# Performance work log

Measured on AMD Instinct MI355X. Metric: run time of the kernel, lower is better.

## Reference

```python
import jax, jax.numpy as jnp
import numpy as np

NS, NI, NC, C, E, M = 50000, 20000, 1000, 128, 1000000, 250000


def setup_inputs() -> dict:
    key = jax.random.key(0)
    ks = jax.random.split(key, 12)
    xavier = (2.0 / (C + C)) ** 0.5  # xavier_normal_ std for square weight
    return {
        "stu_x": jax.random.normal(ks[0], (NS, C), jnp.float32),
        "item_x": jax.random.normal(ks[1], (NI, C), jnp.float32),
        "conc_x": jax.random.normal(ks[2], (NC, C), jnp.float32),
        "W_stu": jax.random.normal(ks[3], (C, C), jnp.float32) * xavier,
        "b_stu": jnp.zeros((C,), jnp.float32),
        "W_item": jax.random.normal(ks[4], (C, C), jnp.float32) * xavier,
        "b_item": jnp.zeros((C,), jnp.float32),
        "W_pred": jax.random.normal(ks[5], (1, C), jnp.float32) * ((2.0 / (1 + C)) ** 0.5),
        "b_pred": jnp.zeros((1,), jnp.float32),
        "stu_track": jax.random.randint(ks[6], (E,), 0, NS, jnp.int32),
        "item_index": jax.random.randint(ks[7], (E,), 0, NI, jnp.int32),
        "conc_index": jax.random.randint(ks[8], (E,), 0, NC, jnp.int32),
        "mean_index": jax.random.randint(ks[9], (E,), 0, M, jnp.int32),
        "num_segments": M,
    }


def _segment_mean(vals, seg_ids, num_segments):
    sums = jax.ops.segment_sum(vals, seg_ids, num_segments=num_segments)
    cnt = jax.ops.segment_sum(jnp.ones((vals.shape[0], 1), vals.dtype), seg_ids,
                              num_segments=num_segments)
    return sums / jnp.maximum(cnt, 1.0)


def reference(stu_x, item_x, conc_x, W_stu, b_stu, W_item, b_item, W_pred, b_pred,
              stu_track, item_index, conc_index, mean_index, num_segments):
    # Feature (stu): shared lin_l=lin_r; aggregate is identity -> per-edge output
    conc_s = conc_x @ W_stu.T          # [NC, C] projected source (concepts)
    stu_p = stu_x @ W_stu.T            # [NS, C] projected target (students)
    stu_feature = jax.nn.sigmoid(conc_s[conc_index] + stu_p[stu_track] + b_stu)  # [E, C]

    # Feature (item): SparseTensor(row=item, col=conc) -> x_j from conc, x_i from item
    conc_i = conc_x @ W_item.T         # [NC, C]
    item_p = item_x @ W_item.T         # [NI, C]
    item_feature = jax.nn.sigmoid(conc_i[conc_index] + item_p[item_index] + b_item)  # [E, C]

    # scatter-mean of per-edge difference over mean_index groups
    pred_input = _segment_mean(stu_feature - item_feature, mean_index, num_segments)  # [M, C]
    pred = jax.nn.sigmoid(pred_input @ W_pred.T + b_pred)  # [M, 1]
    return pred.reshape(-1)
```

## Files before the change

kernel.cpp:

```cpp
#include <hip/hip_runtime.h>

typedef unsigned short u16;
typedef unsigned int   u32;

typedef short short8 __attribute__((ext_vector_type(8)));
typedef float floatx4 __attribute__((ext_vector_type(4)));

#define CDIM 128
#define K_NEG_LOG2E -1.4426950408889634f
#define CNT_SCALE 16777216.0

__device__ __forceinline__ float bf2f_lo(u32 h) {
    union { u32 u; float f; } v; v.u = h << 16; return v.f;
}
__device__ __forceinline__ float bf2f_hi(u32 h) {
    union { u32 u; float f; } v; v.u = h & 0xffff0000u; return v.f;
}
__device__ __forceinline__ u16 f2bf(float f) {
    union { float f; u32 u; } v; v.f = f;
    u32 u = v.u;
    return (u16)((u + 0x7FFFu + ((u >> 16) & 1u)) >> 16);
}
__device__ __forceinline__ float sig_std(float x) {
    return __builtin_amdgcn_rcpf(1.0f + __builtin_amdgcn_exp2f(x * K_NEG_LOG2E));
}

__global__ __launch_bounds__(256) void prep_kernel(
    const float* __restrict__ Wstu, const float* __restrict__ Witem,
    u32* __restrict__ Wbf_pair, float4* __restrict__ zero4, int nZero4,
    const int* __restrict__ stu_track, const int* __restrict__ item_index,
    const int* __restrict__ conc_index, const int* __restrict__ mean_index,
    int4* __restrict__ idx4, int E)
{
    const int tid = blockIdx.x * blockDim.x + threadIdx.x;
    const int stride = gridDim.x * blockDim.x;
    for (int i = tid; i < 16384; i += stride) {
        const float* W = (i & 8192) ? (Witem - 16384) : Wstu;
        const int j = i * 2;
        u32 lo = f2bf(W[j]     * K_NEG_LOG2E);
        u32 hi = f2bf(W[j + 1] * K_NEG_LOG2E);
        Wbf_pair[i] = lo | (hi << 16);
    }
    const float4 z = {0.f, 0.f, 0.f, 0.f};
    for (int i = tid; i < nZero4; i += stride) zero4[i] = z;
    for (int e = tid; e < E; e += stride) {
        int4 t;
        t.x = stu_track[e]  << 8;
        t.y = item_index[e] << 8;
        t.z = conc_index[e] << 9;
        t.w = mean_index[e] << 3;
        idx4[e] = t;
    }
}

__device__ __forceinline__ void proj_tile32(
    const float* __restrict__ X, const u16* __restrict__ Wbf,
    const float* __restrict__ bias, u16* __restrict__ out,
    int nrows, int ostride, int ooff, int row0, int lane)
{
    const int m = lane & 15;
    const int g = lane >> 4;

    short8 a[2][4];
#pragma unroll
    for (int t = 0; t < 2; ++t) {
        int arow = row0 + t * 16 + m;
        if (arow >= nrows) arow = nrows - 1;
        const float* xrow = X + (size_t)arow * CDIM;
#pragma unroll
        for (int s = 0; s < 4; ++s) {
            float4 f0 = *(const float4*)(xrow + s * 32 + g * 8);
            float4 f1 = *(const float4*)(xrow + s * 32 + g * 8 + 4);
            a[t][s][0] = (short)f2bf(f0.x); a[t][s][1] = (short)f2bf(f0.y);
            a[t][s][2] = (short)f2bf(f0.z); a[t][s][3] = (short)f2bf(f0.w);
            a[t][s][4] = (short)f2bf(f1.x); a[t][s][5] = (short)f2bf(f1.y);
            a[t][s][6] = (short)f2bf(f1.z); a[t][s][7] = (short)f2bf(f1.w);
        }
    }

#pragma unroll
    for (int ct = 0; ct < 8; ++ct) {
        const u16* wrow = Wbf + (size_t)(ct * 16 + m) * CDIM;
        floatx4 acc0 = {0.f, 0.f, 0.f, 0.f};
        floatx4 acc1 = {0.f, 0.f, 0.f, 0.f};
#pragma unroll
        for (int s = 0; s < 4; ++s) {
            short8 b = *(const short8*)(wrow + s * 32 + g * 8);
            acc0 = __builtin_amdgcn_mfma_f32_16x16x32_bf16(a[0][s], b, acc0, 0, 0, 0);
            acc1 = __builtin_amdgcn_mfma_f32_16x16x32_bf16(a[1][s], b, acc1, 0, 0, 0);
        }
        const int col = ct * 16 + m;
        const float badd = bias ? bias[col] * K_NEG_LOG2E : 0.f;
#pragma unroll
        for (int i = 0; i < 4; ++i) {
            int r0 = row0 + g * 4 + i;
            if (r0 < nrows)
                out[(size_t)r0 * ostride + ooff + col] =
                    f2bf(__builtin_amdgcn_exp2f(acc0[i] + badd));
            int r1 = r0 + 16;
            if (r1 < nrows)
                out[(size_t)r1 * ostride + ooff + col] =
                    f2bf(__builtin_amdgcn_exp2f(acc1[i] + badd));
        }
    }
}

__global__ __launch_bounds__(256) void proj4_kernel(
    const float* __restrict__ stu_x, const float* __restrict__ item_x,
    const float* __restrict__ conc_x,
    const u16* __restrict__ Wstu_bf, const u16* __restrict__ Witem_bf,
    const float* __restrict__ b_stu, const float* __restrict__ b_item,
    u16* __restrict__ stu_p, u16* __restrict__ item_p, u16* __restrict__ conc_cat,
    int NS, int NI, int NC)
{
    const int lane = threadIdx.x & 63;
    int w = blockIdx.x * 4 + (threadIdx.x >> 6);
    const int T0 = (NS + 31) / 32, T1 = (NI + 31) / 32, T2 = (NC + 31) / 32;

    if (w < T0) { proj_tile32(stu_x, Wstu_bf, nullptr, stu_p, NS, 128, 0, w * 32, lane); return; }
    w -= T0;
    if (w < T1) { proj_tile32(item_x, Witem_bf, nullptr, item_p, NI, 128, 0, w * 32, lane); return; }
    w -= T1;
    if (w < T2) { proj_tile32(conc_x, Wstu_bf, b_stu, conc_cat, NC, 256, 0, w * 32, lane); return; }
    w -= T2;
    if (w < T2) { proj_tile32(conc_x, Witem_bf, b_item, conc_cat, NC, 256, 128, w * 32, lane); return; }
}

__global__ __launch_bounds__(256) void edge_kernel(
    const u16* __restrict__ stu_p, const u16* __restrict__ item_p,
    const u16* __restrict__ conc_cat,
    const int4* __restrict__ idx4,
    const float* __restrict__ w_pred,
    double* __restrict__ sc, int E)
{
    const int lane = threadIdx.x & 63;
    const int sub  = lane & 15;
    const int g    = lane >> 4;
    const int waveId = (int)((blockIdx.x * blockDim.x + threadIdx.x) >> 6);
    const int S      = (int)((gridDim.x * blockDim.x) >> 6);

    const float4 wA = ((const float4*)w_pred)[sub * 2];
    const float4 wB = ((const float4*)w_pred)[sub * 2 + 1];
    float2 w2[4];
    w2[0] = make_float2(wA.x, wA.y); w2[1] = make_float2(wA.z, wA.w);
    w2[2] = make_float2(wB.x, wB.y); w2[3] = make_float2(wB.z, wB.w);
    const u32 lane_off = (u32)sub * 16;

    const int nQuads = (E + 3) >> 2;
    int q = waveId;
    if (q >= nQuads) return;

    auto ldidx = [&](int qq) -> int4 {
        int e = qq * 4 + g;
        e = (e < E) ? e : (E - 1);
        return idx4[e];
    };
    auto compute = [&](const uint4& sv, const uint4& iv,
                       const uint4& ca, const uint4& cb,
                       const int4& I, int qq) {
        const u32 su[4] = {sv.x, sv.y, sv.z, sv.w};
        const u32 iu[4] = {iv.x, iv.y, iv.z, iv.w};
        const u32 au[4] = {ca.x, ca.y, ca.z, ca.w};
        const u32 bu[4] = {cb.x, cb.y, cb.z, cb.w};
        const float2 one = make_float2(1.f, 1.f);
        float2 vacc = make_float2(0.f, 0.f);
#pragma unroll
        for (int j = 0; j < 4; ++j) {
            float2 A  = make_float2(bf2f_lo(au[j]), bf2f_hi(au[j]));
            float2 Sx = make_float2(bf2f_lo(su[j]), bf2f_hi(su[j]));
            float2 B  = make_float2(bf2f_lo(bu[j]), bf2f_hi(bu[j]));
            float2 Ix = make_float2(bf2f_lo(iu[j]), bf2f_hi(iu[j]));
            float2 ea = A * Sx;
            float2 eb = B * Ix;
            float2 den = (ea + one) * (eb + one);
            float2 num = eb - ea;
            float2 rd = make_float2(__builtin_amdgcn_rcpf(den.x),
                                    __builtin_amdgcn_rcpf(den.y));
            vacc += (num * rd) * w2[j];
        }
        float v = vacc.x + vacc.y;
        v += __shfl_xor(v, 1, 64);
        v += __shfl_xor(v, 2, 64);
        v += __shfl_xor(v, 4, 64);
        v += __shfl_xor(v, 8, 64);
        if (sub == 0 && (qq * 4 + g) < E)
            atomicAdd((double*)((char*)sc + (u32)I.w), (double)v + CNT_SCALE);
    };

#define GATH(I_, sv_, iv_, ca_, cb_) { \
        sv_ = *(const uint4*)((const char*)stu_p  + ((u32)(I_).x + lane_off)); \
        iv_ = *(const uint4*)((const char*)item_p + ((u32)(I_).y + lane_off)); \
        const char* cp_ = (const char*)conc_cat + ((u32)(I_).z + lane_off); \
        ca_ = *(const uint4*)cp_; cb_ = *(const uint4*)(cp_ + 256); }

#define STEP(DA, DB, IA, IB, IC) { \
        GATH(I##IB, sv##DB, iv##DB, ca##DB, cb##DB); \
        I##IC = ldidx(q + 2 * S); \
        __builtin_amdgcn_sched_barrier(0); \
        compute(sv##DA, iv##DA, ca##DA, cb##DA, I##IA, q); \
        q += S; \
        if (q >= nQuads) break; }

    int4 I0 = ldidx(q), I1 = ldidx(q + S), I2, I3;
    uint4 sv0, iv0, ca0, cb0, sv1, iv1, ca1, cb1;
    GATH(I0, sv0, iv0, ca0, cb0);

    for (;;) {
        STEP(0, 1, 0, 1, 2)
        STEP(1, 0, 1, 2, 3)
        STEP(0, 1, 2, 3, 0)
        STEP(1, 0, 3, 0, 1)
    }
#undef STEP
#undef GATH
}

__global__ __launch_bounds__(256) void final_kernel(
    const double* __restrict__ sc,
    const float* __restrict__ b_pred, float* __restrict__ out, int M)
{
    const int i = blockIdx.x * blockDim.x + threadIdx.x;
    if (i < M) {
        const double acc = sc[i];
        const double cnt = rint(acc * (1.0 / CNT_SCALE));
        const double sum = acc - cnt * CNT_SCALE;
        const float mean = (float)(sum / fmax(cnt, 1.0));
        out[i] = sig_std(mean + b_pred[0]);
    }
}

extern "C" void kernel_launch(void* const* d_in, const int* in_sizes, int n_in,
                              void* d_out, int out_size, void* d_ws, size_t ws_size,
                              hipStream_t stream) {
    const float* stu_x    = (const float*)d_in[0];
    const float* item_x   = (const float*)d_in[1];
    const float* conc_x   = (const float*)d_in[2];
    const float* W_stu    = (const float*)d_in[3];
    const float* b_stu    = (const float*)d_in[4];
    const float* W_item   = (const float*)d_in[5];
    const float* b_item   = (const float*)d_in[6];
    const float* W_pred   = (const float*)d_in[7];
    const float* b_pred   = (const float*)d_in[8];
    const int* stu_track  = (const int*)d_in[9];
    const int* item_index = (const int*)d_in[10];
    const int* conc_index = (const int*)d_in[11];
    const int* mean_index = (const int*)d_in[12];

    const int NS = in_sizes[0] / CDIM;
    const int NI = in_sizes[1] / CDIM;
    const int NC = in_sizes[2] / CDIM;
    const int E  = in_sizes[9];
    const int M  = out_size;

    double* sc     = (double*)d_ws;
    u16* Wstu_bf   = (u16*)(sc + M);
    u16* Witem_bf  = Wstu_bf + CDIM * CDIM;
    u16* stu_p     = Witem_bf + CDIM * CDIM;
    u16* item_p    = stu_p  + (size_t)NS * CDIM;
    u16* conc_cat  = item_p + (size_t)NI * CDIM;
    int4* idx4     = (int4*)(conc_cat + (size_t)NC * 256);

    const int nZero4 = (int)(((size_t)M * sizeof(double)) / 16);
    prep_kernel<<<1024, 256, 0, stream>>>(W_stu, W_item, (u32*)Wstu_bf,
                                          (float4*)sc, nZero4,
                                          stu_track, item_index, conc_index,
                                          mean_index, idx4, E);

    const int T0 = (NS + 31) / 32, T1 = (NI + 31) / 32, T2 = (NC + 31) / 32;
    const int totalWaves = T0 + T1 + 2 * T2;
    proj4_kernel<<<(totalWaves + 3) / 4, 256, 0, stream>>>(
        stu_x, item_x, conc_x, Wstu_bf, Witem_bf, b_stu, b_item,
        stu_p, item_p, conc_cat, NS, NI, NC);

    edge_kernel<<<4096, 256, 0, stream>>>(stu_p, item_p, conc_cat,
                                          idx4, W_pred, sc, E);

    final_kernel<<<(M + 255) / 256, 256, 0, stream>>>(sc, b_pred, (float*)d_out, M);
}
```

Before: 196.7 us.

## Bucket-sort edges by Morton key of student/item block for gather locality

Edges are counting-sorted into 4096 buckets keyed by interleaved bits of the student and item row blocks. This takes a histogram pass, a prefix scan and a scatter pass, and the scattered order is written into idx4 so the edge kernel visits edges with nearby student and item rows close together in time, aiming for better L2 reuse of the projected-row gathers. The edge kernel grid also drops from 4096 to 1024 blocks, and the scheduling barrier mask is relaxed. The cost is two extra kernel launches, a memset and extra index traffic, and the atomic order in the scatter makes the edge order nondeterministic.

```diff
diff --git a/kernel.cpp b/kernel.cpp
--- a/kernel.cpp
+++ b/kernel.cpp
@@ -9,6 +9,7 @@
 #define CDIM 128
 #define K_NEG_LOG2E -1.4426950408889634f
 #define CNT_SCALE 16777216.0
+#define NBUCK 4096
 
 __device__ __forceinline__ float bf2f_lo(u32 h) {
     union { u32 u; float f; } v; v.u = h << 16; return v.f;
@@ -24,13 +25,21 @@
 __device__ __forceinline__ float sig_std(float x) {
     return __builtin_amdgcn_rcpf(1.0f + __builtin_amdgcn_exp2f(x * K_NEG_LOG2E));
 }
+__device__ __forceinline__ u32 mkey(u32 si, u32 ii) {
+    u32 a = si >> 10, b = ii >> 9, k = 0;
+#pragma unroll
+    for (int i = 0; i < 6; ++i) {
+        k |= ((a >> i) & 1u) << (2 * i + 1);
+        k |= ((b >> i) & 1u) << (2 * i);
+    }
+    return k;
+}
 
 __global__ __launch_bounds__(256) void prep_kernel(
     const float* __restrict__ Wstu, const float* __restrict__ Witem,
     u32* __restrict__ Wbf_pair, float4* __restrict__ zero4, int nZero4,
     const int* __restrict__ stu_track, const int* __restrict__ item_index,
-    const int* __restrict__ conc_index, const int* __restrict__ mean_index,
-    int4* __restrict__ idx4, int E)
+    u32* __restrict__ bucket_cnt, int E)
 {
     const int tid = blockIdx.x * blockDim.x + threadIdx.x;
     const int stride = gridDim.x * blockDim.x;
@@ -43,13 +52,67 @@
     }
     const float4 z = {0.f, 0.f, 0.f, 0.f};
     for (int i = tid; i < nZero4; i += stride) zero4[i] = z;
-    for (int e = tid; e < E; e += stride) {
+    for (int e = tid; e < E; e += stride)
+        atomicAdd(&bucket_cnt[mkey((u32)stu_track[e], (u32)item_index[e])], 1u);
+}
+
+__global__ __launch_bounds__(256) void prefix_kernel(
+    const u32* __restrict__ cnt, u32* __restrict__ cursor)
+{
+    __shared__ u32 psum[256];
+    const int t = threadIdx.x;
+    const int PER = NBUCK / 256;
+    u32 s = 0;
+#pragma unroll
+    for (int j = 0; j < PER; ++j) s += cnt[t * PER + j];
+    psum[t] = s;
+    __syncthreads();
+    for (int off = 1; off < 256; off <<= 1) {
+        u32 add = (t >= off) ? psum[t - off] : 0;
+        __syncthreads();
+        psum[t] += add;
+        __syncthreads();
+    }
+    u32 run = (t > 0) ? psum[t - 1] : 0;
+#pragma unroll
+    for (int j = 0; j < PER; ++j) {
+        cursor[t * PER + j] = run;
+        run += cnt[t * PER + j];
+    }
+}
+
+__global__ __launch_bounds__(256) void scatter_kernel(
+    const int* __restrict__ stu_track, const int* __restrict__ item_index,
+    const int* __restrict__ conc_index, const int* __restrict__ mean_index,
+    u32* __restrict__ cursor, int4* __restrict__ idx4, int E)
+{
+    __shared__ u32 lhist[NBUCK];
+    __shared__ u32 lbase[NBUCK];
+    const int chunk = (E + gridDim.x - 1) / gridDim.x;
+    const int start = blockIdx.x * chunk;
+    const int end   = min(E, start + chunk);
+
+    for (int k = threadIdx.x; k < NBUCK; k += blockDim.x) lhist[k] = 0;
+    __syncthreads();
+    for (int e = start + threadIdx.x; e < end; e += blockDim.x)
+        atomicAdd(&lhist[mkey((u32)stu_track[e], (u32)item_index[e])], 1u);
+    __syncthreads();
+    for (int k = threadIdx.x; k < NBUCK; k += blockDim.x) {
+        const u32 c = lhist[k];
+        lbase[k] = c ? atomicAdd(&cursor[k], c) : 0u;
+        lhist[k] = 0;
+    }
+    __syncthreads();
+    for (int e = start + threadIdx.x; e < end; e += blockDim.x) {
+        const u32 si = (u32)stu_track[e], ii = (u32)item_index[e];
+        const u32 k = mkey(si, ii);
+        const u32 pos = lbase[k] + atomicAdd(&lhist[k], 1u);
         int4 t;
-        t.x = stu_track[e]  << 8;
-        t.y = item_index[e] << 8;
+        t.x = (int)(si << 8);
+        t.y = (int)(ii << 8);
         t.z = conc_index[e] << 9;
         t.w = mean_index[e] << 3;
-        idx4[e] = t;
+        idx4[pos] = t;
     }
 }
 
@@ -157,7 +220,7 @@
     };
     auto compute = [&](const uint4& sv, const uint4& iv,
                        const uint4& ca, const uint4& cb,
-                       const int4& I, int qq) {
+                       int mw, int qq) {
         const u32 su[4] = {sv.x, sv.y, sv.z, sv.w};
         const u32 iu[4] = {iv.x, iv.y, iv.z, iv.w};
         const u32 au[4] = {ca.x, ca.y, ca.z, ca.w};
@@ -184,7 +247,7 @@
         v += __shfl_xor(v, 4, 64);
         v += __shfl_xor(v, 8, 64);
         if (sub == 0 && (qq * 4 + g) < E)
-            atomicAdd((double*)((char*)sc + (u32)I.w), (double)v + CNT_SCALE);
+            atomicAdd((double*)((char*)sc + (u32)mw), (double)v + CNT_SCALE);
     };
 
 #define GATH(I_, sv_, iv_, ca_, cb_) { \
@@ -196,8 +259,8 @@
 #define STEP(DA, DB, IA, IB, IC) { \
         GATH(I##IB, sv##DB, iv##DB, ca##DB, cb##DB); \
         I##IC = ldidx(q + 2 * S); \
-        __builtin_amdgcn_sched_barrier(0); \
-        compute(sv##DA, iv##DA, ca##DA, cb##DA, I##IA, q); \
+        __builtin_amdgcn_sched_barrier(0x7); \
+        compute(sv##DA, iv##DA, ca##DA, cb##DA, I##IA.w, q); \
         q += S; \
         if (q >= nQuads) break; }
 
@@ -259,12 +322,20 @@
     u16* item_p    = stu_p  + (size_t)NS * CDIM;
     u16* conc_cat  = item_p + (size_t)NI * CDIM;
     int4* idx4     = (int4*)(conc_cat + (size_t)NC * 256);
+    u32* bucket_cnt = (u32*)(idx4 + E);
+    u32* cursor     = bucket_cnt + NBUCK;
+
+    hipMemsetAsync(bucket_cnt, 0, NBUCK * sizeof(u32), stream);
 
     const int nZero4 = (int)(((size_t)M * sizeof(double)) / 16);
     prep_kernel<<<1024, 256, 0, stream>>>(W_stu, W_item, (u32*)Wstu_bf,
                                           (float4*)sc, nZero4,
-                                          stu_track, item_index, conc_index,
-                                          mean_index, idx4, E);
+                                          stu_track, item_index, bucket_cnt, E);
+
+    prefix_kernel<<<1, 256, 0, stream>>>(bucket_cnt, cursor);
+
+    scatter_kernel<<<256, 256, 0, stream>>>(stu_track, item_index, conc_index,
+                                            mean_index, cursor, idx4, E);
 
     const int T0 = (NS + 31) / 32, T1 = (NI + 31) / 32, T2 = (NC + 31) / 32;
     const int totalWaves = T0 + T1 + 2 * T2;
@@ -272,7 +343,7 @@
         stu_x, item_x, conc_x, Wstu_bf, Witem_bf, b_stu, b_item,
         stu_p, item_p, conc_cat, NS, NI, NC);
 
-    edge_kernel<<<4096, 256, 0, stream>>>(stu_p, item_p, conc_cat,
+    edge_kernel<<<1024, 256, 0, stream>>>(stu_p, item_p, conc_cat,
                                           idx4, W_pred, sc, E);
 
     final_kernel<<<(M + 255) / 256, 256, 0, stream>>>(sc, b_pred, (float*)d_out, M);
```

Measured after the change: 353.1 us. 79.5% more time.
